# Optimization experiments

Measured on AMD Instinct MI355X. Metric: run time of the kernel, lower is better.

The kernel has to match this reference:

```python
import jax, jax.numpy as jnp
import numpy as np

DIM = 768
HEADS = 12
HEAD_DIM = DIM // HEADS          # 64
DIM_HALF = HEAD_DIM // 2         # 32
SPATIAL = 3


def _rope_cos_sin(grid, voxel_size, theta):
    """grid: static tuple of ints (len SPATIAL); voxel_size: [SPATIAL] float;
    theta: [H, DIM_HALF] per-head frequency spectrum.
    Returns cos, sin of shape [H, N, DIM_HALF] where N = prod(grid)."""
    axes = [jnp.arange(g, dtype=theta.dtype) for g in grid]
    mesh = jnp.meshgrid(*axes, indexing='ij')
    coords = jnp.stack([m.reshape(-1) for m in mesh], axis=-1) * voxel_size  # [N, S] physical coords
    axis_idx = np.arange(DIM_HALF) % len(grid)        # round-robin freq->axis assignment
    pos = coords[:, axis_idx]                          # [N, DIM_HALF]
    ang = pos[None, :, :] * theta[:, None, :]          # [H, N, DIM_HALF]
    return jnp.cos(ang), jnp.sin(ang)


def _rope_apply(t, cos, sin):
    # t: [B, H, N, D]; cos/sin: [H, N, DIM_HALF] broadcast over batch
    t1, t2 = jnp.split(t, 2, axis=-1)
    return jnp.concatenate([t1 * cos - t2 * sin, t1 * sin + t2 * cos], axis=-1)


def setup_inputs() -> dict:
    key = jax.random.key(0)
    k_x, k_qkv, k_proj, k_b = jax.random.split(key, 4)
    B, N = 2, 8 * 16 * 16
    x = jax.random.normal(k_x, (B, N, DIM), dtype=jnp.float32)
    voxel_size = jnp.ones((SPATIAL,), dtype=jnp.float32)
    # nn.Linear weights are [out_features, in_features]
    w_qkv = jax.random.normal(k_qkv, (3 * DIM, DIM), dtype=jnp.float32) * (DIM ** -0.5)
    w_proj = jax.random.normal(k_proj, (DIM, DIM), dtype=jnp.float32) * (DIM ** -0.5)
    b_proj = jax.random.normal(k_b, (DIM,), dtype=jnp.float32) * 0.02
    # learnable per-head base frequencies: theta_j = 10000^{-j/dim_half}
    base = (1.0 / (10000.0 ** (np.arange(DIM_HALF, dtype=np.float32) / DIM_HALF)))
    theta = jnp.asarray(np.tile(base[None, :], (HEADS, 1)))  # [H, DIM_HALF]
    return {"x": x, "voxel_size": voxel_size, "w_qkv": w_qkv, "w_proj": w_proj,
            "b_proj": b_proj, "theta": theta, "grid_d": 8, "grid_h": 16, "grid_w": 16}


def reference(x, voxel_size, w_qkv, w_proj, b_proj, theta, grid_d, grid_h, grid_w):
    B, N, dim = x.shape
    H, D = HEADS, HEAD_DIM
    qkv = jnp.einsum('bnd,ed->bne', x, w_qkv).reshape(B, N, 3, H, D)
    qkv = jnp.transpose(qkv, (2, 0, 3, 1, 4))           # [3, B, H, N, D]
    q, k, v = qkv[0], qkv[1], qkv[2]
    cos, sin = _rope_cos_sin((grid_d, grid_h, grid_w), voxel_size, theta)
    q = _rope_apply(q, cos, sin)
    k = _rope_apply(k, cos, sin)
    scale = 1.0 / np.sqrt(D).astype(np.float32)
    attn = jax.nn.softmax(jnp.einsum('bhnd,bhmd->bhnm', q, k) * scale, axis=-1)
    out = jnp.einsum('bhnm,bhmd->bhnd', attn, v)        # [B, H, N, D]
    out = jnp.transpose(out, (0, 2, 1, 3)).reshape(B, N, dim)
    return out @ w_proj.T + b_proj
```

## Files before the change

kernel.cpp:

```cpp
#include <hip/hip_runtime.h>
#include <stdint.h>

#define DIM 768
#define NHEADS 12
#define HDIM 64
#define DHALF 32
#define NTOK 2048
#define LOG2E 1.44269504088896340736f

typedef unsigned short u16;
typedef unsigned int u32;
typedef __bf16 bf16x8 __attribute__((ext_vector_type(8)));
typedef short s16x8 __attribute__((ext_vector_type(8)));
typedef float f32x4 __attribute__((ext_vector_type(4)));

__device__ __forceinline__ f32x4 f4zero() { f32x4 z = {0.f, 0.f, 0.f, 0.f}; return z; }

__device__ __forceinline__ u16 f2bf(float f) {
    u32 u = __builtin_bit_cast(u32, f);
    u32 r = (u + 0x7FFFu + ((u >> 16) & 1u)) >> 16;
    return (u16)r;
}

__device__ __forceinline__ void gld_lds16(void* lds, const void* g) {
    __builtin_amdgcn_global_load_lds((const __attribute__((address_space(1))) u32*)g,
                                     (__attribute__((address_space(3))) u32*)lds,
                                     16, 0, 0);
}

__global__ __launch_bounds__(256) void cast3_f32_to_bf16(const float* __restrict__ a, u16* __restrict__ oa, int na4,
                                                         const float* __restrict__ b, u16* __restrict__ ob, int nb4,
                                                         const float* __restrict__ c, u16* __restrict__ oc, int nc4) {
    int i = blockIdx.x * 256 + threadIdx.x;
    const float* src;
    u16* dst;
    int j = i;
    if (i < na4) { src = a; dst = oa; }
    else if (i < na4 + nb4) { src = b; dst = ob; j = i - na4; }
    else if (i < na4 + nb4 + nc4) { src = c; dst = oc; j = i - na4 - nb4; }
    else return;
    float4 v = ((const float4*)src)[j];
    u32 w0 = (u32)f2bf(v.x) | ((u32)f2bf(v.y) << 16);
    u32 w1 = (u32)f2bf(v.z) | ((u32)f2bf(v.w) << 16);
    ((uint2*)dst)[j] = make_uint2(w0, w1);
}

__global__ __launch_bounds__(256) void gemm_bt(const u16* __restrict__ A, const u16* __restrict__ Bm,
                                               float* __restrict__ C, const float* __restrict__ bias,
                                               int M, int N, int K) {
    __shared__ __align__(16) u16 sA[128 * 32];
    __shared__ __align__(16) u16 sB[128 * 32];
    const int t = threadIdx.x;
    const int wave = t >> 6, lane = t & 63;
    const int quad = lane >> 4, l16 = lane & 15;
    const int bm = blockIdx.y * 128, bn = blockIdx.x * 128;
    const int wr = wave >> 1, wc = wave & 1;

    f32x4 acc[4][4];
#pragma unroll
    for (int i = 0; i < 4; i++)
#pragma unroll
        for (int j = 0; j < 4; j++) acc[i][j] = f4zero();

    for (int k0 = 0; k0 < K; k0 += 32) {
#pragma unroll
        for (int r = 0; r < 2; ++r) {
            int c = (r * 4 + wave) * 64 + lane;
            int row = c >> 2, kc = c & 3;
            gld_lds16((char*)sA + (size_t)(r * 4 + wave) * 1024,
                      A + (size_t)(bm + row) * K + k0 + kc * 8);
            gld_lds16((char*)sB + (size_t)(r * 4 + wave) * 1024,
                      Bm + (size_t)(bn + row) * K + k0 + kc * 8);
        }
        __syncthreads();
        bf16x8 af[4], bfr[4];
#pragma unroll
        for (int mb = 0; mb < 4; mb++)
            af[mb] = *(const bf16x8*)(sA + (wr * 64 + mb * 16 + l16) * 32 + quad * 8);
#pragma unroll
        for (int nb = 0; nb < 4; nb++)
            bfr[nb] = *(const bf16x8*)(sB + (wc * 64 + nb * 16 + l16) * 32 + quad * 8);
#pragma unroll
        for (int mb = 0; mb < 4; mb++)
#pragma unroll
            for (int nb = 0; nb < 4; nb++)
                acc[mb][nb] = __builtin_amdgcn_mfma_f32_16x16x32_bf16(af[mb], bfr[nb], acc[mb][nb], 0, 0, 0);
        __syncthreads();
    }
#pragma unroll
    for (int mb = 0; mb < 4; mb++)
#pragma unroll
        for (int nb = 0; nb < 4; nb++) {
            int col = bn + wc * 64 + nb * 16 + l16;
            float bv = bias ? bias[col] : 0.f;
#pragma unroll
            for (int r = 0; r < 4; r++) {
                int row = bm + wr * 64 + mb * 16 + quad * 4 + r;
                C[(size_t)row * N + col] = acc[mb][nb][r] + bv;
            }
        }
}

__global__ __launch_bounds__(256) void prep(const float* __restrict__ qkv,
                                            const float* __restrict__ voxel,
                                            const float* __restrict__ theta,
                                            const int* __restrict__ gh_p, const int* __restrict__ gw_p,
                                            u16* __restrict__ q_s, u16* __restrict__ k_s,
                                            u16* __restrict__ vT, int B, int nrope) {
    __shared__ u16 tile[64][66];
    int bid = blockIdx.x;
    int t = threadIdx.x;
    if (bid < nrope) {
        int tid = bid * 256 + t;
        int d = tid & (DHALF - 1);
        int n = (tid >> 5) & (NTOK - 1);
        int hb = tid >> 16;
        int h = hb % NHEADS;
        int b = hb / NHEADS;
        int gh = *gh_p, gw = *gw_p;
        int xw = n % gw;
        int rem = n / gw;
        int yh = rem % gh;
        int zd = rem / gh;
        int axis = d % 3;
        float coordv = (axis == 0 ? (float)zd : (axis == 1 ? (float)yh : (float)xw)) * voxel[axis];
        float ang = coordv * theta[h * DHALF + d];
        float s, c;
        __sincosf(ang, &s, &c);
        size_t bi = ((size_t)b * NTOK + n) * (3 * DIM);
        const float* qp = qkv + bi + h * HDIM;
        float q1 = qp[d], q2 = qp[d + DHALF];
        float k1 = qp[DIM + d], k2 = qp[DIM + d + DHALF];
        size_t bh = (size_t)b * NHEADS + h;
        size_t bo = (bh * NTOK + n) * HDIM;
        const float qscale = 0.125f * LOG2E;
        q_s[bo + d] = f2bf((q1 * c - q2 * s) * qscale);
        q_s[bo + d + DHALF] = f2bf((q1 * s + q2 * c) * qscale);
        int tile_i = n >> 6, r = n & 63, g = r >> 4, k16 = r & 15;
        int qd = d >> 3, j = d & 7;
        size_t off = bh * NTOK * HDIM + (size_t)tile_i * 4096 +
                     (size_t)(g * 2) * 512 + (qd * 16 + k16) * 8 + j;
        k_s[off] = f2bf(k1 * c - k2 * s);
        k_s[off + 512] = f2bf(k1 * s + k2 * c);
    } else {
        int idx = bid - nrope;
        int nt = idx & 31;
        int rem = idx >> 5;
        int h = rem % NHEADS, b = rem / NHEADS;
        int n_loc = t >> 2, d0 = (t & 3) * 16;
        const float* src = qkv + ((size_t)b * NTOK + nt * 64 + n_loc) * (3 * DIM) + 2 * DIM + h * HDIM + d0;
#pragma unroll
        for (int j = 0; j < 16; j += 4) {
            float4 v = *(const float4*)(src + j);
            tile[n_loc][d0 + j + 0] = f2bf(v.x);
            tile[n_loc][d0 + j + 1] = f2bf(v.y);
            tile[n_loc][d0 + j + 2] = f2bf(v.z);
            tile[n_loc][d0 + j + 3] = f2bf(v.w);
        }
        __syncthreads();
        int db = t >> 6, l = t & 63, q = (t >> 4) & 3, l16 = t & 15;
        int dd = db * 16 + l16;
        size_t bh = (size_t)b * NHEADS + h;
#pragma unroll
        for (int c = 0; c < 2; c++) {
            u32 w[4];
#pragma unroll
            for (int jp = 0; jp < 4; jp++) {
                int jj0 = jp * 2, jj1 = jp * 2 + 1;
                int key0 = c * 32 + (jj0 < 4 ? 4 * q + jj0 : 16 + 4 * q + jj0 - 4);
                int key1 = c * 32 + (jj1 < 4 ? 4 * q + jj1 : 16 + 4 * q + jj1 - 4);
                w[jp] = (u32)tile[key0][dd] | ((u32)tile[key1][dd] << 16);
            }
            u16* dst = vT + ((bh * 64 + (size_t)nt * 2 + c) * 2048 + db * 512 + (size_t)l * 8);
            *(uint4*)dst = make_uint4(w[0], w[1], w[2], w[3]);
        }
    }
}

__global__ __launch_bounds__(256) void flash_attn(const u16* __restrict__ Q, const u16* __restrict__ Kp,
                                                  const u16* __restrict__ Vp, u16* __restrict__ Out, int NBH) {
    int i = blockIdx.x;
    int bh_i = i % NBH;
    int qt = i / NBH;
    int b = bh_i / NHEADS, h = bh_i % NHEADS;
    int t = threadIdx.x, wave = t >> 6, lane = t & 63, quad = lane >> 4, l16 = lane & 15;
    size_t bh = (size_t)b * NHEADS + h;
    const u16* Qb = Q + bh * NTOK * HDIM;
    const u16* Kb = Kp + bh * NTOK * HDIM;
    const u16* Vb = Vp + bh * NTOK * HDIM;

    __shared__ __align__(16) u16 smem[2][8192];

    const int q0 = qt * 128 + wave * 32;
    bf16x8 qf[2][2];
#pragma unroll
    for (int qb = 0; qb < 2; qb++)
#pragma unroll
        for (int kc = 0; kc < 2; kc++)
            qf[qb][kc] = *(const bf16x8*)(Qb + (size_t)(q0 + qb * 16 + l16) * HDIM + kc * 32 + quad * 8);

    s16x8 ov;
#pragma unroll
    for (int j = 0; j < 8; j++) ov[j] = (l16 == 0) ? (short)0x3F80 : (short)0;

    f32x4 o[2][5];
#pragma unroll
    for (int qb = 0; qb < 2; qb++)
#pragma unroll
        for (int db = 0; db < 5; db++) o[qb][db] = f4zero();

    auto stage = [&](int kt, int bi) {
        const u16* Kg = Kb + (size_t)kt * 4096;
        const u16* Vg = Vb + (size_t)kt * 4096;
        u16* buf = &smem[bi][0];
#pragma unroll
        for (int s = 0; s < 2; s++) {
            gld_lds16(buf + (wave * 2 + s) * 512, Kg + (wave * 2 + s) * 512 + lane * 8);
            gld_lds16(buf + 4096 + (wave * 2 + s) * 512, Vg + (wave * 2 + s) * 512 + lane * 8);
        }
    };

    stage(0, 0);
    int cur = 0;
    for (int kt = 0; kt < NTOK / 64; ++kt) {
        __syncthreads();
        if (kt + 1 < NTOK / 64) stage(kt + 1, cur ^ 1);
        const u16* sK = &smem[cur][0];
        const u16* sV = &smem[cur][4096];
#pragma unroll
        for (int c = 0; c < 2; ++c) {
            bf16x8 kf[2][2];
#pragma unroll
            for (int kb2 = 0; kb2 < 2; kb2++)
#pragma unroll
                for (int kc = 0; kc < 2; kc++)
                    kf[kb2][kc] = *(const bf16x8*)(sK + ((c * 2 + kb2) * 2 + kc) * 512 + lane * 8);
            s16x8 bv[4];
#pragma unroll
            for (int db = 0; db < 4; db++)
                bv[db] = *(const s16x8*)(sV + c * 2048 + db * 512 + lane * 8);
#pragma unroll
            for (int qb = 0; qb < 2; qb++) {
                f32x4 st0, st1;
                {
                    f32x4 z = f4zero();
                    z = __builtin_amdgcn_mfma_f32_16x16x32_bf16(kf[0][0], qf[qb][0], z, 0, 0, 0);
                    st0 = __builtin_amdgcn_mfma_f32_16x16x32_bf16(kf[0][1], qf[qb][1], z, 0, 0, 0);
                    f32x4 z2 = f4zero();
                    z2 = __builtin_amdgcn_mfma_f32_16x16x32_bf16(kf[1][0], qf[qb][0], z2, 0, 0, 0);
                    st1 = __builtin_amdgcn_mfma_f32_16x16x32_bf16(kf[1][1], qf[qb][1], z2, 0, 0, 0);
                }
                bf16x8 pb;
#pragma unroll
                for (int r = 0; r < 4; r++) {
                    pb[r] = (__bf16)__builtin_exp2f(st0[r]);
                    pb[r + 4] = (__bf16)__builtin_exp2f(st1[r]);
                }
#pragma unroll
                for (int db = 0; db < 4; db++)
                    o[qb][db] = __builtin_amdgcn_mfma_f32_16x16x32_bf16(pb, __builtin_bit_cast(bf16x8, bv[db]),
                                                                       o[qb][db], 0, 0, 0);
                o[qb][4] = __builtin_amdgcn_mfma_f32_16x16x32_bf16(pb, __builtin_bit_cast(bf16x8, ov),
                                                                  o[qb][4], 0, 0, 0);
            }
        }
        cur ^= 1;
    }

#pragma unroll
    for (int qb = 0; qb < 2; qb++)
#pragma unroll
        for (int r = 0; r < 4; r++) {
            float s = __shfl(o[qb][4][r], lane & 48);
            float inv = 1.0f / s;
            int n = q0 + qb * 16 + quad * 4 + r;
            u16* dst = Out + ((size_t)b * NTOK + n) * DIM + h * HDIM + l16;
#pragma unroll
            for (int db = 0; db < 4; db++)
                dst[db * 16] = f2bf(o[qb][db][r] * inv);
        }
}

extern "C" void kernel_launch(void* const* d_in, const int* in_sizes, int n_in,
                              void* d_out, int out_size, void* d_ws, size_t ws_size,
                              hipStream_t stream) {
    const float* x = (const float*)d_in[0];
    const float* voxel = (const float*)d_in[1];
    const float* w_qkv = (const float*)d_in[2];
    const float* w_proj = (const float*)d_in[3];
    const float* b_proj = (const float*)d_in[4];
    const float* theta = (const float*)d_in[5];
    const int* gh_p = (const int*)d_in[7];
    const int* gw_p = (const int*)d_in[8];
    const int B = in_sizes[0] / (NTOK * DIM);
    const int M = B * NTOK;

    char* p = (char*)d_ws;
    u16* xb = (u16*)p;       p += (size_t)M * DIM * 2;
    u16* wqkvb = (u16*)p;    p += (size_t)3 * DIM * DIM * 2;
    u16* wprojb = (u16*)p;   p += (size_t)DIM * DIM * 2;
    float* qkv = (float*)p;  p += (size_t)M * 3 * DIM * 4;
    u16* q_s = (u16*)p;      p += (size_t)M * DIM * 2;
    u16* k_s = (u16*)p;      p += (size_t)M * DIM * 2;
    u16* vT = (u16*)p;       p += (size_t)M * DIM * 2;
    u16* attn = (u16*)p;     p += (size_t)M * DIM * 2;

    int na4 = M * DIM / 4, nb4 = 3 * DIM * DIM / 4, nc4 = DIM * DIM / 4;
    cast3_f32_to_bf16<<<dim3((na4 + nb4 + nc4 + 255) / 256), 256, 0, stream>>>(
        x, xb, na4, w_qkv, wqkvb, nb4, w_proj, wprojb, nc4);

    gemm_bt<<<dim3(3 * DIM / 128, M / 128), 256, 0, stream>>>(xb, wqkvb, qkv, nullptr, M, 3 * DIM, DIM);

    int nrope = (B * NHEADS * NTOK * DHALF) / 256;
    int nvt = B * NHEADS * (NTOK / 64);
    prep<<<dim3(nrope + nvt), 256, 0, stream>>>(qkv, voxel, theta, gh_p, gw_p, q_s, k_s, vT, B, nrope);

    flash_attn<<<dim3((B * NHEADS * NTOK) / 128), 256, 0, stream>>>(q_s, k_s, vT, attn, B * NHEADS);

    gemm_bt<<<dim3(DIM / 128, M / 128), 256, 0, stream>>>(attn, wprojb, (float*)d_out, b_proj, M, DIM, DIM);
}
```

Before: 204.6 us.

## Split attention keys into two halves with a separate combine kernel

Each flash attention block now processes half of the key sequence, which doubles the grid from 384 to 768 blocks so more of the GPU's compute units stay busy. Unnormalized fp32 partial outputs and row sums are written into the reused qkv workspace, and a new combine kernel adds the two halves, normalizes them and writes bf16. The softmax has no running max, so the two partials can simply be added. The cost is extra global traffic for the fp32 partials and one more kernel launch.

New measurement: 195.4 us. 4.5% less time.

```diff
diff --git a/kernel.cpp b/kernel.cpp
--- a/kernel.cpp
+++ b/kernel.cpp
@@ -178,10 +178,13 @@
 }
 
 __global__ __launch_bounds__(256) void flash_attn(const u16* __restrict__ Q, const u16* __restrict__ Kp,
-                                                  const u16* __restrict__ Vp, u16* __restrict__ Out, int NBH) {
+                                                  const u16* __restrict__ Vp, float* __restrict__ Opart,
+                                                  float* __restrict__ Sums, int NBH) {
     int i = blockIdx.x;
     int bh_i = i % NBH;
-    int qt = i / NBH;
+    int rest = i / NBH;
+    int qt = rest >> 1;
+    int ks = rest & 1;
     int b = bh_i / NHEADS, h = bh_i % NHEADS;
     int t = threadIdx.x, wave = t >> 6, lane = t & 63, quad = lane >> 4, l16 = lane & 15;
     size_t bh = (size_t)b * NHEADS + h;
@@ -220,11 +223,13 @@
         }
     };
 
-    stage(0, 0);
+    const int kt0 = ks * (NTOK / 128);
+    const int kt1 = kt0 + (NTOK / 128);
+    stage(kt0, 0);
     int cur = 0;
-    for (int kt = 0; kt < NTOK / 64; ++kt) {
+    for (int kt = kt0; kt < kt1; ++kt) {
         __syncthreads();
-        if (kt + 1 < NTOK / 64) stage(kt + 1, cur ^ 1);
+        if (kt + 1 < kt1) stage(kt + 1, cur ^ 1);
         const u16* sK = &smem[cur][0];
         const u16* sV = &smem[cur][4096];
 #pragma unroll
@@ -267,18 +272,39 @@
         cur ^= 1;
     }
 
+    float* Ob = Opart + ((size_t)ks * NBH + bh) * NTOK * HDIM;
+    float* Sb = Sums + (size_t)ks * NBH * NTOK + bh * NTOK;
 #pragma unroll
     for (int qb = 0; qb < 2; qb++)
 #pragma unroll
         for (int r = 0; r < 4; r++) {
-            float s = __shfl(o[qb][4][r], lane & 48);
-            float inv = 1.0f / s;
             int n = q0 + qb * 16 + quad * 4 + r;
-            u16* dst = Out + ((size_t)b * NTOK + n) * DIM + h * HDIM + l16;
+            if (l16 == 0) Sb[n] = o[qb][4][r];
+            float* dst = Ob + (size_t)n * HDIM + l16;
 #pragma unroll
             for (int db = 0; db < 4; db++)
-                dst[db * 16] = f2bf(o[qb][db][r] * inv);
-        }
+                dst[db * 16] = o[qb][db][r];
+        }
+}
+
+__global__ __launch_bounds__(256) void combine(const float* __restrict__ Opart, const float* __restrict__ Sums,
+                                               u16* __restrict__ attn, int NBH) {
+    int idx = blockIdx.x * 256 + threadIdx.x;
+    int d4 = idx & 15;
+    int n = (idx >> 4) & (NTOK - 1);
+    int bh = idx >> 15;
+    if (bh >= NBH) return;
+    size_t base = ((size_t)bh * NTOK + n) * HDIM + d4 * 4;
+    size_t stride = (size_t)NBH * NTOK * HDIM;
+    float4 a = *(const float4*)(Opart + base);
+    float4 bq = *(const float4*)(Opart + stride + base);
+    float s = Sums[(size_t)bh * NTOK + n] + Sums[(size_t)NBH * NTOK + bh * NTOK + n];
+    float inv = 1.0f / s;
+    int b = bh / NHEADS, h = bh % NHEADS;
+    u16* dst = attn + ((size_t)b * NTOK + n) * DIM + h * HDIM + d4 * 4;
+    u32 w0 = (u32)f2bf((a.x + bq.x) * inv) | ((u32)f2bf((a.y + bq.y) * inv) << 16);
+    u32 w1 = (u32)f2bf((a.z + bq.z) * inv) | ((u32)f2bf((a.w + bq.w) * inv) << 16);
+    *(uint2*)dst = make_uint2(w0, w1);
 }
 
 extern "C" void kernel_launch(void* const* d_in, const int* in_sizes, int n_in,
@@ -294,6 +320,7 @@
     const int* gw_p = (const int*)d_in[8];
     const int B = in_sizes[0] / (NTOK * DIM);
     const int M = B * NTOK;
+    const int NBH = B * NHEADS;
 
     char* p = (char*)d_ws;
     u16* xb = (u16*)p;       p += (size_t)M * DIM * 2;
@@ -305,6 +332,9 @@
     u16* vT = (u16*)p;       p += (size_t)M * DIM * 2;
     u16* attn = (u16*)p;     p += (size_t)M * DIM * 2;
 
+    float* opart = qkv;
+    float* sums = qkv + (size_t)2 * NBH * NTOK * HDIM;
+
     int na4 = M * DIM / 4, nb4 = 3 * DIM * DIM / 4, nc4 = DIM * DIM / 4;
     cast3_f32_to_bf16<<<dim3((na4 + nb4 + nc4 + 255) / 256), 256, 0, stream>>>(
         x, xb, na4, w_qkv, wqkvb, nb4, w_proj, wprojb, nc4);
@@ -315,7 +345,9 @@
     int nvt = B * NHEADS * (NTOK / 64);
     prep<<<dim3(nrope + nvt), 256, 0, stream>>>(qkv, voxel, theta, gh_p, gw_p, q_s, k_s, vT, B, nrope);
 
-    flash_attn<<<dim3((B * NHEADS * NTOK) / 128), 256, 0, stream>>>(q_s, k_s, vT, attn, B * NHEADS);
+    flash_attn<<<dim3(NBH * 32), 256, 0, stream>>>(q_s, k_s, vT, opart, sums, NBH);
+
+    combine<<<dim3(NBH * NTOK * 16 / 256), 256, 0, stream>>>(opart, sums, attn, NBH);
 
     gemm_bt<<<dim3(DIM / 128, M / 128), 256, 0, stream>>>(attn, wprojb, (float*)d_out, b_proj, M, DIM, DIM);
 }
```

## Split flash attention over two key halves with atomic last-block combine

Applied to the files above, without the earlier changes.

Each (batch, head, query tile) is now handled by two blocks, each covering half the key range. Both write unnormalised partial outputs and row sums to a float workspace that reuses the qkv buffer. An atomic flag lets whichever block finishes second add its partner's partial, normalise, and write the bf16 output. This doubles the grid (384 to 768 blocks) to improve occupancy across CUs, at the cost of extra fp32 partial traffic, a memset, and fences. MFMA sections are also wrapped in s_setprio to raise wave priority during matrix work.

New measurement: 339.9 us. +66.1%, slower.

```diff
diff --git a/kernel.cpp b/kernel.cpp
--- a/kernel.cpp
+++ b/kernel.cpp
@@ -178,10 +178,14 @@
 }
 
 __global__ __launch_bounds__(256) void flash_attn(const u16* __restrict__ Q, const u16* __restrict__ Kp,
-                                                  const u16* __restrict__ Vp, u16* __restrict__ Out, int NBH) {
-    int i = blockIdx.x;
-    int bh_i = i % NBH;
-    int qt = i / NBH;
+                                                  const u16* __restrict__ Vp, float* __restrict__ Opart,
+                                                  float* __restrict__ Sums, u16* __restrict__ Out,
+                                                  u32* __restrict__ flags, int NBH) {
+    int bid = blockIdx.x;
+    int g = bid >> 4, j = bid & 7, ks = (bid >> 3) & 1;
+    int u = g * 8 + j;
+    int bh_i = u % NBH;
+    int qt = u / NBH;
     int b = bh_i / NHEADS, h = bh_i % NHEADS;
     int t = threadIdx.x, wave = t >> 6, lane = t & 63, quad = lane >> 4, l16 = lane & 15;
     size_t bh = (size_t)b * NHEADS + h;
@@ -201,7 +205,7 @@
 
     s16x8 ov;
 #pragma unroll
-    for (int j = 0; j < 8; j++) ov[j] = (l16 == 0) ? (short)0x3F80 : (short)0;
+    for (int jj = 0; jj < 8; jj++) ov[jj] = (l16 == 0) ? (short)0x3F80 : (short)0;
 
     f32x4 o[2][5];
 #pragma unroll
@@ -220,11 +224,13 @@
         }
     };
 
-    stage(0, 0);
+    const int kt0 = ks * (NTOK / 128);
+    const int kt1 = kt0 + (NTOK / 128);
+    stage(kt0, 0);
     int cur = 0;
-    for (int kt = 0; kt < NTOK / 64; ++kt) {
+    for (int kt = kt0; kt < kt1; ++kt) {
         __syncthreads();
-        if (kt + 1 < NTOK / 64) stage(kt + 1, cur ^ 1);
+        if (kt + 1 < kt1) stage(kt + 1, cur ^ 1);
         const u16* sK = &smem[cur][0];
         const u16* sV = &smem[cur][4096];
 #pragma unroll
@@ -242,6 +248,7 @@
 #pragma unroll
             for (int qb = 0; qb < 2; qb++) {
                 f32x4 st0, st1;
+                __builtin_amdgcn_s_setprio(1);
                 {
                     f32x4 z = f4zero();
                     z = __builtin_amdgcn_mfma_f32_16x16x32_bf16(kf[0][0], qf[qb][0], z, 0, 0, 0);
@@ -250,34 +257,61 @@
                     z2 = __builtin_amdgcn_mfma_f32_16x16x32_bf16(kf[1][0], qf[qb][0], z2, 0, 0, 0);
                     st1 = __builtin_amdgcn_mfma_f32_16x16x32_bf16(kf[1][1], qf[qb][1], z2, 0, 0, 0);
                 }
+                __builtin_amdgcn_s_setprio(0);
                 bf16x8 pb;
 #pragma unroll
                 for (int r = 0; r < 4; r++) {
                     pb[r] = (__bf16)__builtin_exp2f(st0[r]);
                     pb[r + 4] = (__bf16)__builtin_exp2f(st1[r]);
                 }
+                __builtin_amdgcn_s_setprio(1);
 #pragma unroll
                 for (int db = 0; db < 4; db++)
                     o[qb][db] = __builtin_amdgcn_mfma_f32_16x16x32_bf16(pb, __builtin_bit_cast(bf16x8, bv[db]),
                                                                        o[qb][db], 0, 0, 0);
                 o[qb][4] = __builtin_amdgcn_mfma_f32_16x16x32_bf16(pb, __builtin_bit_cast(bf16x8, ov),
                                                                   o[qb][4], 0, 0, 0);
+                __builtin_amdgcn_s_setprio(0);
             }
         }
         cur ^= 1;
     }
 
+    float* Ob = Opart + ((size_t)ks * NBH + bh) * NTOK * HDIM;
+    float* Sb = Sums + ((size_t)ks * NBH + bh) * NTOK;
 #pragma unroll
     for (int qb = 0; qb < 2; qb++)
 #pragma unroll
         for (int r = 0; r < 4; r++) {
-            float s = __shfl(o[qb][4][r], lane & 48);
+            int n = q0 + qb * 16 + quad * 4 + r;
+            if (l16 == 0) Sb[n] = o[qb][4][r];
+            float* dst = Ob + (size_t)n * HDIM + l16;
+#pragma unroll
+            for (int db = 0; db < 4; db++)
+                dst[db * 16] = o[qb][db][r];
+        }
+    __threadfence();
+    __shared__ int lastflag;
+    __syncthreads();
+    if (t == 0) lastflag = (int)atomicAdd(&flags[u], 1u);
+    __syncthreads();
+    if (lastflag == 0) return;
+    __threadfence();
+
+    const float* Po = Opart + ((size_t)(ks ^ 1) * NBH + bh) * NTOK * HDIM;
+    const float* Ps = Sums + ((size_t)(ks ^ 1) * NBH + bh) * NTOK;
+#pragma unroll
+    for (int qb = 0; qb < 2; qb++)
+#pragma unroll
+        for (int r = 0; r < 4; r++) {
+            int n = q0 + qb * 16 + quad * 4 + r;
+            float s = __shfl(o[qb][4][r], lane & 48) + Ps[n];
             float inv = 1.0f / s;
-            int n = q0 + qb * 16 + quad * 4 + r;
-            u16* dst = Out + ((size_t)b * NTOK + n) * DIM + h * HDIM + l16;
+            const float* psrc = Po + (size_t)n * HDIM + l16;
+            u16* dstb = Out + ((size_t)b * NTOK + n) * DIM + h * HDIM + l16;
 #pragma unroll
             for (int db = 0; db < 4; db++)
-                dst[db * 16] = f2bf(o[qb][db][r] * inv);
+                dstb[db * 16] = f2bf((o[qb][db][r] + psrc[db * 16]) * inv);
         }
 }
 
@@ -294,6 +328,7 @@
     const int* gw_p = (const int*)d_in[8];
     const int B = in_sizes[0] / (NTOK * DIM);
     const int M = B * NTOK;
+    const int NBH = B * NHEADS;
 
     char* p = (char*)d_ws;
     u16* xb = (u16*)p;       p += (size_t)M * DIM * 2;
@@ -304,6 +339,10 @@
     u16* k_s = (u16*)p;      p += (size_t)M * DIM * 2;
     u16* vT = (u16*)p;       p += (size_t)M * DIM * 2;
     u16* attn = (u16*)p;     p += (size_t)M * DIM * 2;
+    u32* flags = (u32*)p;    p += (size_t)NBH * 16 * 4;
+
+    float* opart = qkv;
+    float* sums = qkv + (size_t)2 * NBH * NTOK * HDIM;
 
     int na4 = M * DIM / 4, nb4 = 3 * DIM * DIM / 4, nc4 = DIM * DIM / 4;
     cast3_f32_to_bf16<<<dim3((na4 + nb4 + nc4 + 255) / 256), 256, 0, stream>>>(
@@ -315,7 +354,9 @@
     int nvt = B * NHEADS * (NTOK / 64);
     prep<<<dim3(nrope + nvt), 256, 0, stream>>>(qkv, voxel, theta, gh_p, gw_p, q_s, k_s, vT, B, nrope);
 
-    flash_attn<<<dim3((B * NHEADS * NTOK) / 128), 256, 0, stream>>>(q_s, k_s, vT, attn, B * NHEADS);
+    hipMemsetAsync(flags, 0, (size_t)NBH * 16 * 4, stream);
+
+    flash_attn<<<dim3(NBH * 32), 256, 0, stream>>>(q_s, k_s, vT, opart, sums, attn, flags, NBH);
 
     gemm_bt<<<dim3(DIM / 128, M / 128), 256, 0, stream>>>(attn, wprojb, (float*)d_out, b_proj, M, DIM, DIM);
 }
```
